# Kernel optimization log

Hardware: AMD Instinct MI355X
Metric: run time of the kernel (lower is better)

## Reference

```python
import jax, jax.numpy as jnp
import numpy as np

N_NODES = 100000
N_EDGES = 1600000
D_IN = 64
D_HID = 64
D_OUT = 64


def setup_inputs() -> dict:
    key = jax.random.key(0)
    ks = jax.random.split(key, 12)
    x = jax.random.normal(ks[0], (N_NODES, D_IN), dtype=jnp.float32)
    edge_index = jax.random.randint(ks[1], (2, N_EDGES), 0, N_NODES, dtype=jnp.int64)
    batch = jnp.zeros((N_NODES,), dtype=jnp.int64)
    # Glorot-ish init for GCNConv weights; PyG stores weight as [in, out] applied as x @ W.
    def lin(k, din, dout):
        s = 1.0 / np.sqrt(din)
        return jax.random.uniform(k, (din, dout), minval=-s, maxval=s, dtype=jnp.float32)
    W1 = lin(ks[2], D_IN, D_HID);  b1 = jnp.zeros((D_HID,), jnp.float32)
    W2 = lin(ks[3], D_HID, D_HID); b2 = jnp.zeros((D_HID,), jnp.float32)
    W3 = lin(ks[4], D_HID, D_HID); b3 = jnp.zeros((D_HID,), jnp.float32)
    W4 = lin(ks[5], D_HID, D_OUT); b4 = jnp.zeros((D_OUT,), jnp.float32)
    return {"x": x, "edge_index": edge_index, "batch": batch,
            "W1": W1, "b1": b1, "W2": W2, "b2": b2,
            "W3": W3, "b3": b3, "W4": W4, "b4": b4}


def reference(x, edge_index, batch, W1, b1, W2, b2, W3, b3, W4, b4):
    N = x.shape[0]
    loops = jnp.arange(N, dtype=edge_index.dtype)
    src = jnp.concatenate([edge_index[0], loops])  # [E+N]
    dst = jnp.concatenate([edge_index[1], loops])  # [E+N]
    # Symmetric normalization: deg over A + I (in-degree at dst), norm_e = d_src^-1/2 * d_dst^-1/2
    deg = jax.ops.segment_sum(jnp.ones(src.shape, dtype=x.dtype), dst, num_segments=N)
    dis = jnp.where(deg > 0, jax.lax.rsqrt(deg), 0.0)
    norm = (dis[src] * dis[dst])[:, None]  # [E+N, 1]

    def conv(h, W, b):
        h = h @ W                                   # [N, dout]
        msg = h[src] * norm                         # gather + scale, [E+N, dout]
        return jax.ops.segment_sum(msg, dst, num_segments=N) + b

    h = jax.nn.elu(conv(x, W1, b1))   # dropout_p=0.0 -> identity
    h = jax.nn.elu(conv(h, W2, b2))
    h = jax.nn.elu(conv(h, W3, b3))
    return conv(h, W4, b4)
```

## Files before the change

### kernel.cpp

```cpp
#include <hip/hip_runtime.h>

#define NN 100000
#define NE 1600000
#define DD 64
#define BSH 9
#define BSZ 512
#define NBKT 196
#define BCAP 16384
#define CHUNK 8192
#define NCH ((NE + CHUNK - 1) / CHUNK)
#define CSR2_CAP (NE + 16 * NN + 1024)


__global__ void k_zero(int* __restrict__ bcur, int* __restrict__ gcur,
                       float* __restrict__ h2s) {
    int t = threadIdx.x;
    if (t < NBKT) bcur[t] = 0;
    if (t == 255) *gcur = 0;
    if (t < DD) h2s[(size_t)NN * DD + t] = 0.f;
}


__global__ __launch_bounds__(256) void k_bscat(const int* __restrict__ ei,
                                               int* __restrict__ bcur,
                                               int* __restrict__ bkt) {
    __shared__ int h[NBKT], rbase[NBKT], rcur[NBKT];
    int t = threadIdx.x;
    for (int i = t; i < NBKT; i += 256) h[i] = 0;
    __syncthreads();
    int cb = blockIdx.x * CHUNK;
    int s[32], d[32];
#pragma unroll
    for (int i = 0; i < 32; ++i) {
        int e = cb + t + 256 * i;
        if (e < NE) {
            s[i] = ei[e];
            d[i] = ei[NE + e];
            atomicAdd(&h[d[i] >> BSH], 1);
        } else {
            d[i] = -1;
        }
    }
    __syncthreads();
    for (int i = t; i < NBKT; i += 256) {
        int c = h[i];
        rbase[i] = c ? atomicAdd(&bcur[i], c) : 0;
        rcur[i] = 0;
    }
    __syncthreads();
#pragma unroll
    for (int i = 0; i < 32; ++i) {
        if (d[i] >= 0) {
            int b = d[i] >> BSH;
            int pos = rbase[b] + atomicAdd(&rcur[b], 1);
            bkt[(size_t)b * BCAP + pos] = s[i] | ((d[i] & (BSZ - 1)) << 17);
        }
    }
}


__global__ __launch_bounds__(256) void k_merge(const int* __restrict__ bcur,
                                               const int* __restrict__ bkt,
                                               int* __restrict__ gcur,
                                               int* __restrict__ rbeg,
                                               int* __restrict__ rlen,
                                               double* __restrict__ dis,
                                               int* __restrict__ csr2) {
    __shared__ int cnt[BSZ];
    __shared__ int cur[BSZ];
    __shared__ int s2[256];
    __shared__ int sbase;
    int b = blockIdx.x, t = threadIdx.x;
    cnt[t] = 0; cnt[t + 256] = 0;
    __syncthreads();
    int ec = bcur[b];
    const int* row = bkt + (size_t)b * BCAP;
    for (int j = t; j < ec; j += 256)
        atomicAdd(&cnt[row[j] >> 17], 1);
    __syncthreads();
    int nb = b * BSZ;
    int n0 = nb + 2 * t, n1 = nb + 2 * t + 1;
    int c0 = (n0 < NN) ? cnt[2 * t] : -1;
    int c1 = (n1 < NN) ? cnt[2 * t + 1] : -1;
    int q0 = (c0 >= 0) ? ((c0 + 16) & ~15) : 0;
    int q1 = (c1 >= 0) ? ((c1 + 16) & ~15) : 0;
    s2[t] = q0 + q1;
    __syncthreads();
    for (int o = 1; o < 256; o <<= 1) {
        int v = (t >= o) ? s2[t - o] : 0;
        __syncthreads();
        s2[t] += v;
        __syncthreads();
    }
    if (t == 255) sbase = atomicAdd(gcur, s2[255]);
    __syncthreads();
    int base = sbase;
    int ex = s2[t] - (q0 + q1);
    if (c0 >= 0) {
        rbeg[n0] = base + ex; rlen[n0] = q0;
        dis[n0] = 1.0 / sqrt((double)(c0 + 1));
        csr2[base + ex] = n0;
        cur[2 * t] = ex + 1;
    }
    if (c1 >= 0) {
        rbeg[n1] = base + ex + q0; rlen[n1] = q1;
        dis[n1] = 1.0 / sqrt((double)(c1 + 1));
        csr2[base + ex + q0] = n1;
        cur[2 * t + 1] = ex + q0 + 1;
    }
    __syncthreads();
    for (int j = t; j < ec; j += 256) {
        int pk = row[j];
        int pos = base + atomicAdd(&cur[pk >> 17], 1);
        csr2[pos] = pk & 0x1FFFF;
    }
    __syncthreads();
    if (c0 >= 0) { int e0 = ex + q0;      for (int j = cur[2 * t];     j < e0; ++j) csr2[base + j] = NN; }
    if (c1 >= 0) { int e1 = ex + q0 + q1; for (int j = cur[2 * t + 1]; j < e1; ++j) csr2[base + j] = NN; }
}


__global__ __launch_bounds__(256) void k_gemm(const float* __restrict__ in,
                                              const float* __restrict__ W,
                                              const double* __restrict__ dis,
                                              float* __restrict__ h2s) {
    __shared__ float sW[DD * DD];
    __shared__ float sIn[128 * 65];
    int t = threadIdx.x;
    int brow = blockIdx.x * 128;
#pragma unroll
    for (int i = 0; i < 16; ++i) sW[t + 256 * i] = W[t + 256 * i];
#pragma unroll
    for (int i = 0; i < 32; ++i) {
        int idx = t + 256 * i;
        int rr = idx >> 6, kk = idx & 63;
        int gr = brow + rr; if (gr >= NN) gr = NN - 1;
        sIn[rr * 65 + kk] = in[(size_t)gr * DD + kk];
    }
    __syncthreads();
    int cg = t & 7;
    int rg = t >> 3;
    const float* sInB = &sIn[rg * 4 * 65];

    float aE[4][8], aO[4][8];
#pragma unroll
    for (int i = 0; i < 4; ++i)
#pragma unroll
        for (int j = 0; j < 8; ++j) { aE[i][j] = 0.f; aO[i][j] = 0.f; }

#pragma unroll 4
    for (int k = 0; k < DD; k += 2) {
        float4 w0 = *(const float4*)&sW[k * DD + cg * 8];
        float4 w1 = *(const float4*)&sW[k * DD + cg * 8 + 4];
        float4 w2 = *(const float4*)&sW[(k + 1) * DD + cg * 8];
        float4 w3 = *(const float4*)&sW[(k + 1) * DD + cg * 8 + 4];
        float wv0[8] = {w0.x, w0.y, w0.z, w0.w, w1.x, w1.y, w1.z, w1.w};
        float wv1[8] = {w2.x, w2.y, w2.z, w2.w, w3.x, w3.y, w3.z, w3.w};
#pragma unroll
        for (int i = 0; i < 4; ++i) {
            float a0 = sInB[i * 65 + k];
            float a1 = sInB[i * 65 + k + 1];
#pragma unroll
            for (int j = 0; j < 8; ++j) {
                aE[i][j] = fmaf(a0, wv0[j], aE[i][j]);
                aO[i][j] = fmaf(a1, wv1[j], aO[i][j]);
            }
        }
    }

#pragma unroll
    for (int i = 0; i < 4; ++i) {
        int row = brow + rg * 4 + i;
        if (row < NN) {
            double dr = dis[row];
            float o[8];
#pragma unroll
            for (int j = 0; j < 8; ++j)
                o[j] = (float)((double)(aE[i][j] + aO[i][j]) * dr);
            *(float4*)&h2s[(size_t)row * DD + cg * 8]     = make_float4(o[0], o[1], o[2], o[3]);
            *(float4*)&h2s[(size_t)row * DD + cg * 8 + 4] = make_float4(o[4], o[5], o[6], o[7]);
        }
    }
}


__global__ __launch_bounds__(256) void k_aggr(const int* __restrict__ rbeg,
                                              const int* __restrict__ rlen,
                                              const int* __restrict__ csr2,
                                              const float* __restrict__ h2s,
                                              const double* __restrict__ dis,
                                              const float* __restrict__ b,
                                              float* __restrict__ out,
                                              int apply_elu) {
    int gid = blockIdx.x * 256 + threadIdx.x;
    int node = gid >> 6;
    int lane = gid & 63;
    int beg = __builtin_amdgcn_readfirstlane(rbeg[node]);
    int end = beg + __builtin_amdgcn_readfirstlane(rlen[node]);
    double a0 = 0.0, a1 = 0.0, a2 = 0.0, a3 = 0.0;
    for (int j = beg; j < end; j += 16) {
        int4 i0 = *(const int4*)&csr2[j];
        int4 i1 = *(const int4*)&csr2[j + 4];
        int4 i2 = *(const int4*)&csr2[j + 8];
        int4 i3 = *(const int4*)&csr2[j + 12];
        float v0  = h2s[(size_t)(unsigned)i0.x * DD + lane];
        float v1  = h2s[(size_t)(unsigned)i0.y * DD + lane];
        float v2  = h2s[(size_t)(unsigned)i0.z * DD + lane];
        float v3  = h2s[(size_t)(unsigned)i0.w * DD + lane];
        float v4  = h2s[(size_t)(unsigned)i1.x * DD + lane];
        float v5  = h2s[(size_t)(unsigned)i1.y * DD + lane];
        float v6  = h2s[(size_t)(unsigned)i1.z * DD + lane];
        float v7  = h2s[(size_t)(unsigned)i1.w * DD + lane];
        float v8  = h2s[(size_t)(unsigned)i2.x * DD + lane];
        float v9  = h2s[(size_t)(unsigned)i2.y * DD + lane];
        float v10 = h2s[(size_t)(unsigned)i2.z * DD + lane];
        float v11 = h2s[(size_t)(unsigned)i2.w * DD + lane];
        float v12 = h2s[(size_t)(unsigned)i3.x * DD + lane];
        float v13 = h2s[(size_t)(unsigned)i3.y * DD + lane];
        float v14 = h2s[(size_t)(unsigned)i3.z * DD + lane];
        float v15 = h2s[(size_t)(unsigned)i3.w * DD + lane];
        a0 += (double)v0;  a1 += (double)v1;  a2 += (double)v2;  a3 += (double)v3;
        a0 += (double)v4;  a1 += (double)v5;  a2 += (double)v6;  a3 += (double)v7;
        a0 += (double)v8;  a1 += (double)v9;  a2 += (double)v10; a3 += (double)v11;
        a0 += (double)v12; a1 += (double)v13; a2 += (double)v14; a3 += (double)v15;
    }
    double sum = (a0 + a1) + (a2 + a3);
    float vf = (float)(dis[node] * sum + (double)b[lane]);
    if (apply_elu && vf <= 0.f) vf = expm1f(vf);
    out[gid] = vf;
}


static inline size_t align256(size_t x) { return (x + 255) & ~(size_t)255; }

extern "C" void kernel_launch(void* const* d_in, const int* in_sizes, int n_in,
                              void* d_out, int out_size, void* d_ws, size_t ws_size,
                              hipStream_t stream) {
    const float* x  = (const float*)d_in[0];
    const int*   ei = (const int*)d_in[1];
    const float* W1 = (const float*)d_in[3];
    const float* b1 = (const float*)d_in[4];
    const float* W2 = (const float*)d_in[5];
    const float* b2 = (const float*)d_in[6];
    const float* W3 = (const float*)d_in[7];
    const float* b3 = (const float*)d_in[8];
    const float* W4 = (const float*)d_in[9];
    const float* b4 = (const float*)d_in[10];
    float* out = (float*)d_out;

    char* ws = (char*)d_ws;
    size_t off = 0;
    float*  h2s  = (float*) (ws + off); off = align256(off + (size_t)(NN + 1) * DD * sizeof(float));
    float*  A    = (float*) (ws + off); off = align256(off + (size_t)NN * DD * sizeof(float));
    double* dis  = (double*)(ws + off); off = align256(off + (size_t)NN * sizeof(double));
    int*    rbeg = (int*)   (ws + off); off = align256(off + (size_t)NN * sizeof(int));
    int*    rlen = (int*)   (ws + off); off = align256(off + (size_t)NN * sizeof(int));
    int*    bcur = (int*)   (ws + off); off = align256(off + (size_t)(NBKT + 1) * sizeof(int));
    int*    gcur = (int*)   (ws + off); off = align256(off + 256 * sizeof(int));
    int*    bkt  = (int*)   (ws + off); off = align256(off + (size_t)NBKT * BCAP * sizeof(int));
    int*    csr2 = (int*)   (ws + off); off = align256(off + (size_t)CSR2_CAP * sizeof(int));

    k_zero <<<1, 256, 0, stream>>>(bcur, gcur, h2s);
    k_bscat<<<NCH, 256, 0, stream>>>(ei, bcur, bkt);
    k_merge<<<NBKT, 256, 0, stream>>>(bcur, bkt, gcur, rbeg, rlen, dis, csr2);

    struct Layer { const float* in; const float* W; const float* b; float* o; int elu; };
    Layer L[4] = {
        { x,   W1, b1, A,   1 },
        { A,   W2, b2, out, 1 },
        { out, W3, b3, A,   1 },
        { A,   W4, b4, out, 0 },
    };

    const int NGB = (NN + 127) / 128;
    for (int l = 0; l < 4; ++l) {
        k_gemm<<<NGB, 256, 0, stream>>>(L[l].in, L[l].W, dis, h2s);
        k_aggr<<<NN / 4, 256, 0, stream>>>(rbeg, rlen, csr2, h2s, dis,
                                           L[l].b, L[l].o, L[l].elu);
    }
}
```

Baseline: 370.3 us.

## Restructure GEMM kernel to hold weight column in registers with broadcast LDS rows

The dense transform kernel now keeps one full column of W (64 floats) in registers per thread and reads input rows from shared memory as broadcast float4 loads. Each thread computes one output column for 16 rows, with 64-row tiles per block instead of 128. This removes the shared-memory copy of W and the padded input tile, cutting LDS traffic and footprint. The cost is higher register pressure, four partial sums per output that change the floating-point summation order, and scalar instead of float4 output stores.

```diff
diff --git a/kernel.cpp b/kernel.cpp
--- a/kernel.cpp
+++ b/kernel.cpp
@@ -124,61 +124,44 @@
                                               const float* __restrict__ W,
                                               const double* __restrict__ dis,
                                               float* __restrict__ h2s) {
-    __shared__ float sW[DD * DD];
-    __shared__ float sIn[128 * 65];
+    __shared__ float sIn[64 * 64];
     int t = threadIdx.x;
-    int brow = blockIdx.x * 128;
-#pragma unroll
-    for (int i = 0; i < 16; ++i) sW[t + 256 * i] = W[t + 256 * i];
-#pragma unroll
-    for (int i = 0; i < 32; ++i) {
-        int idx = t + 256 * i;
-        int rr = idx >> 6, kk = idx & 63;
+    int brow = blockIdx.x * 64;
+    int c = t & 63;
+    int w = t >> 6;
+
+    float wk[64];
+#pragma unroll
+    for (int k = 0; k < 64; ++k) wk[k] = W[k * DD + c];
+
+#pragma unroll
+    for (int i = 0; i < 4; ++i) {
+        int idx4 = i * 256 + t;
+        int rr = idx4 >> 4, c4 = idx4 & 15;
         int gr = brow + rr; if (gr >= NN) gr = NN - 1;
-        sIn[rr * 65 + kk] = in[(size_t)gr * DD + kk];
-    }
-    __syncthreads();
-    int cg = t & 7;
-    int rg = t >> 3;
-    const float* sInB = &sIn[rg * 4 * 65];
-
-    float aE[4][8], aO[4][8];
-#pragma unroll
-    for (int i = 0; i < 4; ++i)
-#pragma unroll
-        for (int j = 0; j < 8; ++j) { aE[i][j] = 0.f; aO[i][j] = 0.f; }
-
-#pragma unroll 4
-    for (int k = 0; k < DD; k += 2) {
-        float4 w0 = *(const float4*)&sW[k * DD + cg * 8];
-        float4 w1 = *(const float4*)&sW[k * DD + cg * 8 + 4];
-        float4 w2 = *(const float4*)&sW[(k + 1) * DD + cg * 8];
-        float4 w3 = *(const float4*)&sW[(k + 1) * DD + cg * 8 + 4];
-        float wv0[8] = {w0.x, w0.y, w0.z, w0.w, w1.x, w1.y, w1.z, w1.w};
-        float wv1[8] = {w2.x, w2.y, w2.z, w2.w, w3.x, w3.y, w3.z, w3.w};
-#pragma unroll
-        for (int i = 0; i < 4; ++i) {
-            float a0 = sInB[i * 65 + k];
-            float a1 = sInB[i * 65 + k + 1];
-#pragma unroll
-            for (int j = 0; j < 8; ++j) {
-                aE[i][j] = fmaf(a0, wv0[j], aE[i][j]);
-                aO[i][j] = fmaf(a1, wv1[j], aO[i][j]);
-            }
-        }
-    }
-
-#pragma unroll
-    for (int i = 0; i < 4; ++i) {
-        int row = brow + rg * 4 + i;
+        *(float4*)&sIn[rr * 64 + c4 * 4] =
+            *(const float4*)&in[(size_t)gr * DD + c4 * 4];
+    }
+    __syncthreads();
+
+    const float* base = &sIn[(w * 16) * 64];
+#pragma unroll 2
+    for (int r = 0; r < 16; ++r) {
+        const float4* row4 = (const float4*)&base[r * 64];
+        float a0 = 0.f, a1 = 0.f, a2 = 0.f, a3 = 0.f;
+#pragma unroll
+        for (int kb = 0; kb < 16; ++kb) {
+            float4 av = row4[kb];
+            a0 = fmaf(av.x, wk[kb * 4 + 0], a0);
+            a1 = fmaf(av.y, wk[kb * 4 + 1], a1);
+            a2 = fmaf(av.z, wk[kb * 4 + 2], a2);
+            a3 = fmaf(av.w, wk[kb * 4 + 3], a3);
+        }
+        int row = brow + w * 16 + r;
         if (row < NN) {
             double dr = dis[row];
-            float o[8];
-#pragma unroll
-            for (int j = 0; j < 8; ++j)
-                o[j] = (float)((double)(aE[i][j] + aO[i][j]) * dr);
-            *(float4*)&h2s[(size_t)row * DD + cg * 8]     = make_float4(o[0], o[1], o[2], o[3]);
-            *(float4*)&h2s[(size_t)row * DD + cg * 8 + 4] = make_float4(o[4], o[5], o[6], o[7]);
+            h2s[(size_t)row * DD + c] =
+                (float)((double)((a0 + a1) + (a2 + a3)) * dr);
         }
     }
 }
@@ -272,7 +255,7 @@
         { A,   W4, b4, out, 0 },
     };
 
-    const int NGB = (NN + 127) / 128;
+    const int NGB = (NN + 63) / 64;
     for (int l = 0; l < 4; ++l) {
         k_gemm<<<NGB, 256, 0, stream>>>(L[l].in, L[l].W, dis, h2s);
         k_aggr<<<NN / 4, 256, 0, stream>>>(rbeg, rlen, csr2, h2s, dis,
```

Result: slower. 422.1 us (+14.0%).
